# Kernel tuning notes

Measured on AMD Instinct MI355X. Metric: run time of the kernel, lower is better.

## Reference

```python
import math
import jax, jax.numpy as jnp
import numpy as np

B, T, C, HS = 8, 2048, 1024, 64

def setup_inputs() -> dict:
    key = jax.random.key(0)
    kx, kq, kk, kv = jax.random.split(key, 4)
    x = jax.random.normal(kx, (B, T, C), dtype=jnp.float32)
    # match nn.Linear init scale roughly: U(-1/sqrt(C), 1/sqrt(C))
    lim = 1.0 / math.sqrt(C)
    Wq = jax.random.uniform(kq, (C, HS), minval=-lim, maxval=lim, dtype=jnp.float32)
    Wk = jax.random.uniform(kk, (C, HS), minval=-lim, maxval=lim, dtype=jnp.float32)
    Wv = jax.random.uniform(kv, (C, HS), minval=-lim, maxval=lim, dtype=jnp.float32)
    return {"x": x, "Wq": Wq, "Wk": Wk, "Wv": Wv}

def reference(x, Wq, Wk, Wv):
    # NOTE: original scales by 1/sqrt(hs) where hs = x.shape[-1] = embd_size,
    # not head_size. Faithfully reproduced.
    Tlen = x.shape[1]
    scale = 1.0 / math.sqrt(x.shape[-1])
    q = jnp.einsum('btc,ch->bth', x, Wq)
    k = jnp.einsum('btc,ch->bth', x, Wk)
    v = jnp.einsum('btc,ch->bth', x, Wv)
    wei = jnp.einsum('bth,bsh->bts', q, k) * scale  # [B,T,T]
    causal = jnp.tril(jnp.ones((Tlen, Tlen), dtype=bool))
    wei = jnp.where(causal, wei, -jnp.inf)
    wei = jax.nn.softmax(wei, axis=-1)
    # dropout p=0.0 -> identity
    out = jnp.einsum('bts,bsh->bth', wei, v)  # [B,T,HS]
    return out
```

## Files before the change

kernel.cpp:

```cpp
#include <hip/hip_runtime.h>
#include <hip/hip_bf16.h>


#define T_SEQ 2048
#define C_DIM 1024
#define HS 64
#define BT 16384

typedef short s8v __attribute__((ext_vector_type(8)));
typedef float f4v __attribute__((ext_vector_type(4)));

__device__ inline unsigned short f2bf(float f) {
  union { float f; unsigned u; } a; a.f = f;
  unsigned r = a.u + 0x7fffu + ((a.u >> 16) & 1u);
  return (unsigned short)(r >> 16);
}

__device__ inline unsigned pk2(float a, float b) {
  union { __hip_bfloat162 h; unsigned u; } c;
  c.h = __float22bfloat162_rn(make_float2(a, b));
  return c.u;
}

__device__ inline s8v cvt8(float4 v0, float4 v1) {
  union { unsigned u[4]; s8v v; } r;
  r.u[0] = pk2(v0.x, v0.y); r.u[1] = pk2(v0.z, v0.w);
  r.u[2] = pk2(v1.x, v1.y); r.u[3] = pk2(v1.z, v1.w);
  return r.v;
}

__device__ inline void gl_lds16(const void* g, unsigned char* lds_base,
                                unsigned uniform_byte_off) {
  __builtin_amdgcn_global_load_lds(
      (const __attribute__((address_space(1))) unsigned int*)g,
      (__attribute__((address_space(3))) unsigned int*)(lds_base + uniform_byte_off),
      16, 0, 0);
}

__global__ __launch_bounds__(256) void wt_kernel(
    const float* __restrict__ Wq, const float* __restrict__ Wk,
    const float* __restrict__ Wv, unsigned short* __restrict__ wt) {
  __shared__ float tile[64][65];
  const int bid = blockIdx.x;
  const int mat = bid >> 4, kt = bid & 15;
  const float* W = (mat == 0) ? Wq : ((mat == 1) ? Wk : Wv);
  const int t = threadIdx.x;
  const int n = t & 63, kr = t >> 6;
#pragma unroll
  for (int j = 0; j < 16; ++j) {
    const int kl = j * 4 + kr;
    tile[kl][n] = W[(kt * 64 + kl) * HS + n];
  }
  __syncthreads();
  const int n2 = t >> 2, kp = t & 3;
  unsigned int* orow =
      (unsigned int*)(wt + (size_t)(mat * 64 + n2) * C_DIM + kt * 64);
#pragma unroll
  for (int i = 0; i < 8; ++i) {
    const int k0 = kp * 16 + i * 2;
    unsigned int lo = f2bf(tile[k0][n2]);
    unsigned int hi = f2bf(tile[k0 + 1][n2]);
    orow[kp * 8 + i] = lo | (hi << 16);
  }
}

__global__ __launch_bounds__(512) void qkv_kernel(
    const float* __restrict__ x, const unsigned short* __restrict__ wt,
    unsigned short* __restrict__ qws, unsigned short* __restrict__ kws,
    unsigned short* __restrict__ vtws) {
  __shared__ unsigned char abuf[2][16384];
  __shared__ unsigned char bbuf[2][24576];

  const int tid  = threadIdx.x;
  const int wv   = tid >> 6;
  const int lane = tid & 63;
  const int m    = lane & 15;
  const int quad = lane >> 4;
  const int wq = wv & 3, th = wv >> 2;
  const int mh = wq >> 1, ng = (wq & 1) * 6;
  const int row0 = blockIdx.x * 64;

  f4v acc[6];
#pragma unroll
  for (int j = 0; j < 6; ++j) acc[j] = (f4v)0.0f;

  const unsigned au = (unsigned)__builtin_amdgcn_readfirstlane(tid & 448) << 4;

  const float* agp[2];
#pragma unroll
  for (int j = 0; j < 2; ++j) {
    const int s = tid + j * 512;
    const int r = s >> 4, p = (s & 15) ^ (r & 15);
    agp[j] = x + (size_t)(row0 + r) * C_DIM + p * 4;
  }
  const unsigned short* bgp[3];
#pragma unroll
  for (int j = 0; j < 3; ++j) {
    const int s = tid + j * 512;
    const int n = s >> 3, p = (s & 7) ^ (n & 7);
    bgp[j] = wt + (size_t)n * C_DIM + p * 8;
  }

  int aoff[2][2];
#pragma unroll
  for (int c = 0; c < 2; ++c)
#pragma unroll
    for (int t = 0; t < 2; ++t)
      aoff[c][t] =
          (((th * 32 + mh * 16 + m) * 16) + ((c * 8 + 2 * quad + t) ^ m)) << 4;
  int boff[6][2];
#pragma unroll
  for (int j = 0; j < 6; ++j) {
    const int n = (ng + j) * 16 + m;
#pragma unroll
    for (int c = 0; c < 2; ++c)
      boff[j][c] = (n * 8 + ((c * 4 + quad) ^ (n & 7))) << 4;
  }

#define STAGE(buf, kk)                                                       \
  do {                                                                       \
    _Pragma("unroll") for (int j = 0; j < 2; ++j)                            \
        gl_lds16(agp[j] + (kk), abuf[buf], au + (unsigned)(j * 8192));       \
    _Pragma("unroll") for (int j = 0; j < 3; ++j)                            \
        gl_lds16(bgp[j] + (kk), bbuf[buf], au + (unsigned)(j * 8192));       \
  } while (0)

  STAGE(0, 0);
  for (int it = 0; it < 16; ++it) {
    __syncthreads();
    if (it < 15) STAGE((it + 1) & 1, (it + 1) * 64);
    const unsigned char* aB = abuf[it & 1];
    const unsigned char* bB = bbuf[it & 1];
#pragma unroll
    for (int c = 0; c < 2; ++c) {
      float4 xa = *(const float4*)(aB + aoff[c][0]);
      float4 xb = *(const float4*)(aB + aoff[c][1]);
      s8v a = cvt8(xa, xb);
#pragma unroll
      for (int j = 0; j < 6; ++j) {
        s8v b = *(const s8v*)(bB + boff[j][c]);
        acc[j] = __builtin_amdgcn_mfma_f32_16x16x32_bf16(a, b, acc[j], 0, 0, 0);
      }
    }
  }
#undef STAGE

  const float qscale = 1.4426950408889634f / 32.0f;
#pragma unroll
  for (int j = 0; j < 6; ++j) {
    const int nt = ng + j;
    const int mat = nt >> 2, ct = nt & 3;
    const int col = ct * 16 + m;
#pragma unroll
    for (int r = 0; r < 4; ++r) {
      const int row = row0 + th * 32 + mh * 16 + quad * 4 + r;
      const float v = acc[j][r];
      if (mat == 0) {
        qws[row * HS + col] = f2bf(v * qscale);
      } else if (mat == 1) {
        kws[row * HS + col] = f2bf(v);
      } else {
        const int bb = row >> 11, t = row & 2047;
        const int s = t & 63;
        const int jp = (s & 32) | ((s & 12) << 1) | ((s & 16) >> 2) | (s & 3);
        vtws[(bb * HS + col) * T_SEQ + ((t & ~63) | jp)] = f2bf(v);
      }
    }
  }
}

__global__ __launch_bounds__(512) void attn_kernel(
    const unsigned short* __restrict__ qws, const unsigned short* __restrict__ kws,
    const unsigned short* __restrict__ vtws, float* __restrict__ out) {
  __shared__ float mo[8][32][64];
  __shared__ float ml[8][32];

  const int tid  = threadIdx.x;
  const int wv   = tid >> 6;
  const int lane = tid & 63;
  const int m    = lane & 15;
  const int quad = lane >> 4;
  const int b    = blockIdx.x & 7;
  const int pr   = blockIdx.x >> 3;
  const int rS   = pr * 32;
  const int rB   = (63 - pr) * 32;
  const int grS  = b * T_SEQ + rS;
  const int grB  = b * T_SEQ + rB;

  const unsigned short* qpS = qws + (size_t)(grS + m) * HS + quad * 8;
  const unsigned short* qpB = qws + (size_t)(grB + m) * HS + quad * 8;
  s8v aq[4][2];
  aq[0][0] = *(const s8v*)qpS;
  aq[0][1] = *(const s8v*)(qpS + 32);
  aq[1][0] = *(const s8v*)(qpS + 16 * HS);
  aq[1][1] = *(const s8v*)(qpS + 16 * HS + 32);
  aq[2][0] = *(const s8v*)qpB;
  aq[2][1] = *(const s8v*)(qpB + 32);
  aq[3][0] = *(const s8v*)(qpB + 16 * HS);
  aq[3][1] = *(const s8v*)(qpB + 16 * HS + 32);

  float li[4] = {0.f, 0.f, 0.f, 0.f};
  f4v o[4][4];
#pragma unroll
  for (int t = 0; t < 4; ++t)
#pragma unroll
    for (int i = 0; i < 4; ++i) o[t][i] = (f4v)0.0f;

  const int nstS = (rS + 32 + 63) >> 6;
  const int nstB = (rB + 32 + 63) >> 6;
  const int qb0 = rS;
  const int qb1 = rS + 16;
  const int qb2 = rB;
  const int qb3 = rB + 16;
  const unsigned short* kbase = kws + (size_t)b * T_SEQ * HS;
  const unsigned short* vbase = vtws + (size_t)b * HS * T_SEQ;

#define TILE(t, qb)                                                          \
  {                                                                          \
    f4v s_[4];                                                               \
    _Pragma("unroll") for (int ns = 0; ns < 4; ++ns) {                       \
      f4v u_ = (f4v)0.0f;                                                    \
      u_ = __builtin_amdgcn_mfma_f32_16x16x32_bf16(kf[ns][0], aq[t][0], u_, 0, 0, 0); \
      u_ = __builtin_amdgcn_mfma_f32_16x16x32_bf16(kf[ns][1], aq[t][1], u_, 0, 0, 0); \
      s_[ns] = u_;                                                           \
    }                                                                        \
    const int qr_ = (qb) + m;                                                \
    union { unsigned u[4]; s8v v; } paA_, paB_;                              \
    _Pragma("unroll") for (int ns = 0; ns < 4; ++ns) {                       \
      const int sb_ = s0 + ns * 16 + quad * 4;                               \
      const float p0 = (sb_     > qr_) ? 0.f : __builtin_amdgcn_exp2f(s_[ns][0]); \
      const float p1 = (sb_ + 1 > qr_) ? 0.f : __builtin_amdgcn_exp2f(s_[ns][1]); \
      const float p2 = (sb_ + 2 > qr_) ? 0.f : __builtin_amdgcn_exp2f(s_[ns][2]); \
      const float p3 = (sb_ + 3 > qr_) ? 0.f : __builtin_amdgcn_exp2f(s_[ns][3]); \
      li[t] += (p0 + p1) + (p2 + p3);                                        \
      if (ns < 2) {                                                          \
        paA_.u[ns * 2] = pk2(p0, p1); paA_.u[ns * 2 + 1] = pk2(p2, p3);      \
      } else {                                                               \
        paB_.u[(ns - 2) * 2] = pk2(p0, p1);                                  \
        paB_.u[(ns - 2) * 2 + 1] = pk2(p2, p3);                              \
      }                                                                      \
    }                                                                        \
    _Pragma("unroll") for (int hn = 0; hn < 4; ++hn) {                       \
      o[t][hn] = __builtin_amdgcn_mfma_f32_16x16x32_bf16(paA_.v, vf[hn][0], o[t][hn], 0, 0, 0); \
      o[t][hn] = __builtin_amdgcn_mfma_f32_16x16x32_bf16(paB_.v, vf[hn][1], o[t][hn], 0, 0, 0); \
    }                                                                        \
  }

  for (int st = wv; st < nstB; st += 8) {
    const int s0 = st * 64;

    s8v kf[4][2];
#pragma unroll
    for (int ns = 0; ns < 4; ++ns) {
      const unsigned short* kp = &kbase[(size_t)(s0 + ns * 16 + m) * HS + quad * 8];
      kf[ns][0] = *(const s8v*)kp;
      kf[ns][1] = *(const s8v*)(kp + 32);
    }
    s8v vf[4][2];
#pragma unroll
    for (int hn = 0; hn < 4; ++hn) {
      const unsigned short* vp = &vbase[(size_t)(hn * 16 + m) * T_SEQ + s0 + quad * 8];
      vf[hn][0] = *(const s8v*)vp;
      vf[hn][1] = *(const s8v*)(vp + 32);
    }

    const bool low = (st < nstS);
    if (low) { TILE(0, qb0); TILE(1, qb1); }
    TILE(2, qb2);
    TILE(3, qb3);
  }
#undef TILE

#pragma unroll
  for (int t = 0; t < 4; ++t) {
    float s = li[t];
    s += __shfl_xor(s, 16); s += __shfl_xor(s, 32);
    li[t] = s;
  }

  const int row = tid >> 4, c4 = (tid & 15) * 4;
#pragma unroll
  for (int ps = 0; ps < 2; ++ps) {
    __syncthreads();
#pragma unroll
    for (int hn = 0; hn < 4; ++hn)
#pragma unroll
      for (int r = 0; r < 4; ++r) {
        mo[wv][quad * 4 + r][hn * 16 + m]      = o[2 * ps][hn][r];
        mo[wv][16 + quad * 4 + r][hn * 16 + m] = o[2 * ps + 1][hn][r];
      }
    if (quad == 0) {
      ml[wv][m]      = li[2 * ps];
      ml[wv][16 + m] = li[2 * ps + 1];
    }
    __syncthreads();

    float ls = 0.f;
#pragma unroll
    for (int w = 0; w < 8; ++w) ls += ml[w][row];
    const float inv = 1.0f / ls;
    float ax = 0.f, ay = 0.f, az = 0.f, aw = 0.f;
#pragma unroll
    for (int w = 0; w < 8; ++w) {
      float4 v = *(const float4*)&mo[w][row][c4];
      ax += v.x; ay += v.y; az += v.z; aw += v.w;
    }
    const int gr = ps ? grB : grS;
    float4 res;
    res.x = ax * inv; res.y = ay * inv; res.z = az * inv; res.w = aw * inv;
    *(float4*)&out[(size_t)(gr + row) * HS + c4] = res;
  }
}

extern "C" void kernel_launch(void* const* d_in, const int* in_sizes, int n_in,
                              void* d_out, int out_size, void* d_ws, size_t ws_size,
                              hipStream_t stream) {
  const float* x  = (const float*)d_in[0];
  const float* Wq = (const float*)d_in[1];
  const float* Wk = (const float*)d_in[2];
  const float* Wv = (const float*)d_in[3];
  float* out = (float*)d_out;

  unsigned short* qws  = (unsigned short*)d_ws;
  unsigned short* kws  = qws + (size_t)BT * HS;
  unsigned short* vtws = kws + (size_t)BT * HS;
  unsigned short* wt   = vtws + (size_t)BT * HS;

  wt_kernel<<<dim3(48), dim3(256), 0, stream>>>(Wq, Wk, Wv, wt);
  qkv_kernel<<<dim3(BT / 64), dim3(512), 0, stream>>>(x, wt, qws, kws, vtws);
  attn_kernel<<<dim3(256), dim3(512), 0, stream>>>(qws, kws, vtws, out);
}
```

Before: 133.3 us.

## Software-pipeline K/V tile loads with QK^T and PV MFMA phases

Splits each tile's work into separate QK^T/softmax and PV phases. The K and V fragments for the next key tile are prefetched into registers while the current tile's PV MFMAs run, and the first tile is loaded before the loop. This is meant to hide global-load latency behind matrix math instead of stalling at the top of each iteration. It adds live registers for the prefetched fragments and the stored P values, which could lower occupancy, and the last iteration issues a redundant reload.

```diff
diff --git a/kernel.cpp b/kernel.cpp
--- a/kernel.cpp
+++ b/kernel.cpp
@@ -201,6 +201,7 @@
 
   float li[4] = {0.f, 0.f, 0.f, 0.f};
   f4v o[4][4];
+  s8v pa[4][2];
 #pragma unroll
   for (int t = 0; t < 4; ++t)
 #pragma unroll
@@ -215,7 +216,30 @@
   const unsigned short* kbase = kws + (size_t)b * T_SEQ * HS;
   const unsigned short* vbase = vtws + (size_t)b * HS * T_SEQ;
 
-#define TILE(t, qb)                                                          \
+  s8v kf[4][2], vf[4][2];
+
+#define LOADK(stv)                                                           \
+  {                                                                          \
+    const int s0_ = (stv) * 64;                                              \
+    _Pragma("unroll") for (int ns = 0; ns < 4; ++ns) {                       \
+      const unsigned short* kp_ =                                            \
+          &kbase[(size_t)(s0_ + ns * 16 + m) * HS + quad * 8];               \
+      kf[ns][0] = *(const s8v*)kp_;                                          \
+      kf[ns][1] = *(const s8v*)(kp_ + 32);                                   \
+    }                                                                        \
+  }
+#define LOADV(stv)                                                           \
+  {                                                                          \
+    const int s0_ = (stv) * 64;                                              \
+    _Pragma("unroll") for (int hn = 0; hn < 4; ++hn) {                       \
+      const unsigned short* vp_ =                                            \
+          &vbase[(size_t)(hn * 16 + m) * T_SEQ + s0_ + quad * 8];            \
+      vf[hn][0] = *(const s8v*)vp_;                                          \
+      vf[hn][1] = *(const s8v*)(vp_ + 32);                                   \
+    }                                                                        \
+  }
+
+#define QKT(t, qb)                                                           \
   {                                                                          \
     f4v s_[4];                                                               \
     _Pragma("unroll") for (int ns = 0; ns < 4; ++ns) {                       \
@@ -240,36 +264,38 @@
         paB_.u[(ns - 2) * 2 + 1] = pk2(p2, p3);                              \
       }                                                                      \
     }                                                                        \
+    pa[t][0] = paA_.v; pa[t][1] = paB_.v;                                    \
+  }
+
+#define PVT(t)                                                               \
+  {                                                                          \
     _Pragma("unroll") for (int hn = 0; hn < 4; ++hn) {                       \
-      o[t][hn] = __builtin_amdgcn_mfma_f32_16x16x32_bf16(paA_.v, vf[hn][0], o[t][hn], 0, 0, 0); \
-      o[t][hn] = __builtin_amdgcn_mfma_f32_16x16x32_bf16(paB_.v, vf[hn][1], o[t][hn], 0, 0, 0); \
-    }                                                                        \
-  }
-
+      o[t][hn] = __builtin_amdgcn_mfma_f32_16x16x32_bf16(pa[t][0], vf[hn][0], o[t][hn], 0, 0, 0); \
+      o[t][hn] = __builtin_amdgcn_mfma_f32_16x16x32_bf16(pa[t][1], vf[hn][1], o[t][hn], 0, 0, 0); \
+    }                                                                        \
+  }
+
+  LOADK(wv);
+  LOADV(wv);
   for (int st = wv; st < nstB; st += 8) {
     const int s0 = st * 64;
-
-    s8v kf[4][2];
-#pragma unroll
-    for (int ns = 0; ns < 4; ++ns) {
-      const unsigned short* kp = &kbase[(size_t)(s0 + ns * 16 + m) * HS + quad * 8];
-      kf[ns][0] = *(const s8v*)kp;
-      kf[ns][1] = *(const s8v*)(kp + 32);
-    }
-    s8v vf[4][2];
-#pragma unroll
-    for (int hn = 0; hn < 4; ++hn) {
-      const unsigned short* vp = &vbase[(size_t)(hn * 16 + m) * T_SEQ + s0 + quad * 8];
-      vf[hn][0] = *(const s8v*)vp;
-      vf[hn][1] = *(const s8v*)(vp + 32);
-    }
-
     const bool low = (st < nstS);
-    if (low) { TILE(0, qb0); TILE(1, qb1); }
-    TILE(2, qb2);
-    TILE(3, qb3);
-  }
-#undef TILE
+    if (low) {
+      QKT(0, qb0); QKT(1, qb1);
+      PVT(0); PVT(1);
+    }
+    QKT(2, qb2);
+    QKT(3, qb3);
+    const int stn = (st + 8 < nstB) ? st + 8 : st;
+    LOADK(stn);
+    PVT(2);
+    PVT(3);
+    LOADV(stn);
+  }
+#undef QKT
+#undef PVT
+#undef LOADK
+#undef LOADV
 
 #pragma unroll
   for (int t = 0; t < 4; ++t) {
```

New measurement: 137.5 us. 1.03x slower.
